# Performance work log

Measured on AMD Instinct MI355X. Metric: run time of the kernel, lower is better.

The kernel has to match this reference:

```python
import jax, jax.numpy as jnp
import numpy as np

D_MODEL = 1024
D_FF = 2048
NA = 4
NB = 4
E = NA * NB
B = 2
S = 1024


def setup_inputs() -> dict:
    key = jax.random.key(0)
    ks = jax.random.split(key, 8)
    s = 0.02
    x = jax.random.normal(ks[0], (B, S, D_MODEL), dtype=jnp.float32)
    # stacked per-expert FFN params (torch Linear stored as [in, out] here)
    W1 = (jax.random.normal(ks[1], (E, D_MODEL, 2 * D_FF), dtype=jnp.float32) * s)
    b1 = jnp.zeros((E, 2 * D_FF), dtype=jnp.float32)
    W2 = (jax.random.normal(ks[2], (E, D_FF, D_MODEL), dtype=jnp.float32) * s)
    b2 = jnp.zeros((E, D_MODEL), dtype=jnp.float32)
    Wga = jax.random.normal(ks[3], (D_MODEL, NA), dtype=jnp.float32) * s
    bga = jnp.zeros((NA,), dtype=jnp.float32)
    Wgb = jax.random.normal(ks[4], (D_MODEL, NB), dtype=jnp.float32) * s
    bgb = jnp.zeros((NB,), dtype=jnp.float32)
    return {"x": x, "W1": W1, "b1": b1, "W2": W2, "b2": b2,
            "Wga": Wga, "bga": bga, "Wgb": Wgb, "bgb": bgb}


def reference(x, W1, b1, W2, b2, Wga, bga, Wgb, bgb):
    b, s, d = x.shape
    xf = x.reshape(b * s, d)                     # [T, d]
    probs_A = jax.nn.softmax(xf @ Wga + bga, axis=-1)   # [T, NA]
    probs_B = jax.nn.softmax(xf @ Wgb + bgb, axis=-1)   # [T, NB]
    idx_A = jnp.argmax(probs_A, axis=-1)
    idx_B = jnp.argmax(probs_B, axis=-1)
    oh_A = jax.nn.one_hot(idx_A, NA, dtype=xf.dtype)
    oh_B = jax.nn.one_hot(idx_B, NB, dtype=xf.dtype)
    aux_A = NA * jnp.sum(probs_A.mean(0) * oh_A.mean(0))
    aux_B = NB * jnp.sum(probs_B.mean(0) * oh_B.mean(0))
    total_aux = aux_A + aux_B

    # flattened Cartesian expert index per token
    e_idx = idx_A * NB + idx_B                   # [T]

    # run all experts densely, then select per token (vectorized dispatch)
    h = jnp.einsum('td,edf->etf', xf, W1) + b1[:, None, :]   # [E, T, 2*d_ff]
    a, g = jnp.split(h, 2, axis=-1)
    act = a * jax.nn.silu(g)                                  # [E, T, d_ff]
    y = jnp.einsum('etf,efd->etd', act, W2) + b2[:, None, :]  # [E, T, d]
    oh_E = jax.nn.one_hot(e_idx, E, dtype=xf.dtype)           # [T, E]
    out = jnp.einsum('te,etd->td', oh_E, y)                   # [T, d]
    return out.reshape(b, s, d), total_aux
```

## Files before the change

kernel.cpp:

```cpp
#include <hip/hip_runtime.h>
#include <cstdint>
#include <cstddef>

#define TOKENS 2048
#define DM 1024
#define DFF 2048
#define HC 4096
#define NE 16
#define BM 128

typedef __bf16 bf16x8 __attribute__((ext_vector_type(8)));
typedef float floatx4 __attribute__((ext_vector_type(4)));

static __device__ __forceinline__ unsigned short f2bf(float f) {
    union { float f; unsigned int u; } v; v.f = f;
    unsigned int r = v.u + 0x7fffu + ((v.u >> 16) & 1u);
    return (unsigned short)(r >> 16);
}

union BF8 { bf16x8 v; unsigned short u[8]; };

__global__ __launch_bounds__(256) void moe_gating(
    const float* __restrict__ x, const float* __restrict__ Wga, const float* __restrict__ bga,
    const float* __restrict__ Wgb, const float* __restrict__ bgb,
    float* __restrict__ probsA, float* __restrict__ probsB, int* __restrict__ e_idx)
{
    int wv = threadIdx.x >> 6, lane = threadIdx.x & 63;
    int t = blockIdx.x * 4 + wv;
    const float* xr = x + (size_t)t * DM;
    double aA[4] = {0.,0.,0.,0.}, aB[4] = {0.,0.,0.,0.};
    for (int k = lane; k < DM; k += 64) {
        double xv = (double)xr[k];
        float4 wa = *(const float4*)(Wga + k * 4);
        float4 wb = *(const float4*)(Wgb + k * 4);
        aA[0] += xv * wa.x; aA[1] += xv * wa.y; aA[2] += xv * wa.z; aA[3] += xv * wa.w;
        aB[0] += xv * wb.x; aB[1] += xv * wb.y; aB[2] += xv * wb.z; aB[3] += xv * wb.w;
    }
    #pragma unroll
    for (int off = 32; off >= 1; off >>= 1) {
        #pragma unroll
        for (int j = 0; j < 4; ++j) {
            aA[j] += __shfl_xor(aA[j], off);
            aB[j] += __shfl_xor(aB[j], off);
        }
    }
    if (lane == 0) {
        double lA[4], lB[4];
        #pragma unroll
        for (int j = 0; j < 4; ++j) {
            lA[j] = aA[j] + (double)bga[j];
            lB[j] = aB[j] + (double)bgb[j];
        }
        int ia = 0, ib = 0;
        #pragma unroll
        for (int j = 1; j < 4; ++j) {
            if (lA[j] > lA[ia]) ia = j;
            if (lB[j] > lB[ib]) ib = j;
        }
        double sA = 0., sB = 0., pA[4], pB[4];
        #pragma unroll
        for (int j = 0; j < 4; ++j) {
            pA[j] = exp(lA[j] - lA[ia]); sA += pA[j];
            pB[j] = exp(lB[j] - lB[ib]); sB += pB[j];
        }
        float4 oa, ob;
        oa.x = (float)(pA[0]/sA); oa.y = (float)(pA[1]/sA);
        oa.z = (float)(pA[2]/sA); oa.w = (float)(pA[3]/sA);
        ob.x = (float)(pB[0]/sB); ob.y = (float)(pB[1]/sB);
        ob.z = (float)(pB[2]/sB); ob.w = (float)(pB[3]/sB);
        *(float4*)(probsA + t * 4) = oa;
        *(float4*)(probsB + t * 4) = ob;
        e_idx[t] = ia * 4 + ib;
    }
}

__global__ __launch_bounds__(256) void moe_stats(
    const float* __restrict__ probsA, const float* __restrict__ probsB,
    const int* __restrict__ e_idx,
    int* __restrict__ countE, int* __restrict__ offsets, float* __restrict__ aux_out)
{
    __shared__ float sA[4], sB[4];
    __shared__ int cA[4], cB[4], cE[16];
    int tid = threadIdx.x;
    if (tid < 4) { sA[tid] = 0.f; sB[tid] = 0.f; cA[tid] = 0; cB[tid] = 0; }
    if (tid < 16) cE[tid] = 0;
    __syncthreads();
    float lA[4] = {0,0,0,0}, lB[4] = {0,0,0,0};
    for (int t = tid; t < TOKENS; t += 256) {
        float4 pa = *(const float4*)(probsA + t * 4);
        float4 pb = *(const float4*)(probsB + t * 4);
        lA[0] += pa.x; lA[1] += pa.y; lA[2] += pa.z; lA[3] += pa.w;
        lB[0] += pb.x; lB[1] += pb.y; lB[2] += pb.z; lB[3] += pb.w;
        int e = e_idx[t];
        atomicAdd(&cE[e], 1);
        atomicAdd(&cA[e >> 2], 1);
        atomicAdd(&cB[e & 3], 1);
    }
    #pragma unroll
    for (int j = 0; j < 4; ++j) {
        atomicAdd(&sA[j], lA[j]);
        atomicAdd(&sB[j], lB[j]);
    }
    __syncthreads();
    if (tid == 0) {
        int acc = 0;
        for (int e = 0; e < NE; ++e) { offsets[e] = acc; countE[e] = cE[e]; acc += cE[e]; }
        offsets[NE] = acc;
        float invT = 1.0f / (float)TOKENS;
        float auxA = 0.f, auxB = 0.f;
        for (int j = 0; j < 4; ++j) {
            auxA += (sA[j] * invT) * ((float)cA[j] * invT);
            auxB += (sB[j] * invT) * ((float)cB[j] * invT);
        }
        aux_out[0] = 4.0f * auxA + 4.0f * auxB;
    }
}

__global__ __launch_bounds__(256) void moe_slot(const int* __restrict__ e_idx,
                                                const int* __restrict__ offsets,
                                                int* __restrict__ cursor, int* __restrict__ perm)
{
    int t = blockIdx.x * 256 + threadIdx.x;
    int e = e_idx[t];
    int s = offsets[e] + atomicAdd(&cursor[e], 1);
    perm[s] = t;
}

__global__ __launch_bounds__(256) void moe_gather(const float* __restrict__ x,
                                                  const int* __restrict__ perm,
                                                  unsigned short* __restrict__ Xg)
{
    int s = blockIdx.x;
    int t = perm[s];
    int i = threadIdx.x * 4;
    float4 v = *(const float4*)(x + (size_t)t * DM + i);
    ushort4 o;
    o.x = f2bf(v.x); o.y = f2bf(v.y); o.z = f2bf(v.z); o.w = f2bf(v.w);
    *(ushort4*)(Xg + (size_t)s * DM + i) = o;
}

__global__ __launch_bounds__(256) void moe_ffn1(
    const unsigned short* __restrict__ Xg, const float* __restrict__ W1,
    const float* __restrict__ b1, const int* __restrict__ countE,
    const int* __restrict__ offsets, unsigned short* __restrict__ actbuf)
{
    int e = blockIdx.y;
    int cnt = countE[e];
    if (cnt == 0) return;
    int base = offsets[e];
    int n0 = blockIdx.x * 64;
    __shared__ __align__(16) unsigned short Xs[2 * BM * 40];
    int tid = threadIdx.x, wv = tid >> 6, lane = tid & 63;
    int quad = lane >> 4, l15 = lane & 15;
    const float* W1e = W1 + (size_t)e * DM * HC;
    int col = n0 + wv * 16 + l15;
    const float* pa = W1e + col;
    const float* pg = W1e + DFF + col;
    float ba = b1[e * HC + col];
    float bg = b1[e * HC + DFF + col];
    int row = tid >> 2, kc = tid & 3;

    for (int m0 = blockIdx.z * BM; m0 < cnt; m0 += 2 * BM) {
        floatx4 acc[8][2];
        #pragma unroll
        for (int i = 0; i < 8; ++i) {
            acc[i][0] = floatx4{0.f,0.f,0.f,0.f};
            acc[i][1] = floatx4{0.f,0.f,0.f,0.f};
        }
        #pragma unroll
        for (int p = 0; p < 2; ++p) {
            int r = row + p * 64;
            uint4 v = {0u,0u,0u,0u};
            int m = m0 + r;
            if (m < cnt) v = *(const uint4*)(Xg + (size_t)(base + m) * DM + kc * 8);
            *(uint4*)(Xs + r * 40 + kc * 8) = v;
        }
        float curA[8], curG[8], nxtA[8], nxtG[8];
        {
            const float* qa = pa + (size_t)(quad * 8) * HC;
            const float* qg = pg + (size_t)(quad * 8) * HC;
            #pragma unroll
            for (int j = 0; j < 8; ++j) { curA[j] = qa[(size_t)j * HC]; curG[j] = qg[(size_t)j * HC]; }
        }
        __syncthreads();
        for (int ks = 0; ks < DM / 32; ++ks) {
            int buf = ks & 1;
            if (ks + 1 < DM / 32) {
                int k0n = (ks + 1) * 32;
                #pragma unroll
                for (int p = 0; p < 2; ++p) {
                    int r = row + p * 64;
                    uint4 v = {0u,0u,0u,0u};
                    int m = m0 + r;
                    if (m < cnt) v = *(const uint4*)(Xg + (size_t)(base + m) * DM + k0n + kc * 8);
                    *(uint4*)(Xs + (buf ^ 1) * (BM * 40) + r * 40 + kc * 8) = v;
                }
            }
            bf16x8 af[8];
            #pragma unroll
            for (int i = 0; i < 8; ++i)
                af[i] = *(const bf16x8*)(Xs + buf * (BM * 40) + (i * 16 + l15) * 40 + quad * 8);
            if (ks + 1 < DM / 32) {
                const float* qa = pa + (size_t)((ks + 1) * 32 + quad * 8) * HC;
                const float* qg = pg + (size_t)((ks + 1) * 32 + quad * 8) * HC;
                #pragma unroll
                for (int j = 0; j < 8; ++j) { nxtA[j] = qa[(size_t)j * HC]; nxtG[j] = qg[(size_t)j * HC]; }
            }
            BF8 fa, fg;
            #pragma unroll
            for (int j = 0; j < 8; ++j) { fa.u[j] = f2bf(curA[j]); fg.u[j] = f2bf(curG[j]); }
            #pragma unroll
            for (int i = 0; i < 8; ++i) {
                acc[i][0] = __builtin_amdgcn_mfma_f32_16x16x32_bf16(af[i], fa.v, acc[i][0], 0, 0, 0);
                acc[i][1] = __builtin_amdgcn_mfma_f32_16x16x32_bf16(af[i], fg.v, acc[i][1], 0, 0, 0);
            }
            #pragma unroll
            for (int j = 0; j < 8; ++j) { curA[j] = nxtA[j]; curG[j] = nxtG[j]; }
            __syncthreads();
        }
        #pragma unroll
        for (int i = 0; i < 8; ++i) {
            #pragma unroll
            for (int r = 0; r < 4; ++r) {
                int mr = m0 + i * 16 + quad * 4 + r;
                if (mr < cnt) {
                    float a = acc[i][0][r] + ba;
                    float g = acc[i][1][r] + bg;
                    float sg = 1.0f / (1.0f + __expf(-g));
                    actbuf[(size_t)(base + mr) * DFF + col] = f2bf(a * (g * sg));
                }
            }
        }
    }
}

__global__ __launch_bounds__(256) void moe_ffn2(
    const unsigned short* __restrict__ actbuf, const float* __restrict__ W2,
    const float* __restrict__ b2, const int* __restrict__ countE,
    const int* __restrict__ offsets, const int* __restrict__ perm,
    float* __restrict__ out)
{
    int e = blockIdx.y;
    int cnt = countE[e];
    if (cnt == 0) return;
    int base = offsets[e];
    int n0 = blockIdx.x * 64;
    __shared__ __align__(16) unsigned short As[2 * BM * 40];
    int tid = threadIdx.x, wv = tid >> 6, lane = tid & 63;
    int quad = lane >> 4, l15 = lane & 15;
    const float* W2e = W2 + (size_t)e * DFF * DM;
    int col = n0 + wv * 16 + l15;
    const float* pb = W2e + col;
    float bias = b2[e * DM + col];
    int row = tid >> 2, kc = tid & 3;

    for (int m0 = blockIdx.z * BM; m0 < cnt; m0 += 2 * BM) {
        floatx4 acc[8];
        #pragma unroll
        for (int i = 0; i < 8; ++i) acc[i] = floatx4{0.f,0.f,0.f,0.f};
        #pragma unroll
        for (int p = 0; p < 2; ++p) {
            int r = row + p * 64;
            uint4 v = {0u,0u,0u,0u};
            int m = m0 + r;
            if (m < cnt) v = *(const uint4*)(actbuf + (size_t)(base + m) * DFF + kc * 8);
            *(uint4*)(As + r * 40 + kc * 8) = v;
        }
        float curB[8], nxtB[8];
        {
            const float* qb = pb + (size_t)(quad * 8) * DM;
            #pragma unroll
            for (int j = 0; j < 8; ++j) curB[j] = qb[(size_t)j * DM];
        }
        __syncthreads();
        for (int ks = 0; ks < DFF / 32; ++ks) {
            int buf = ks & 1;
            if (ks + 1 < DFF / 32) {
                int k0n = (ks + 1) * 32;
                #pragma unroll
                for (int p = 0; p < 2; ++p) {
                    int r = row + p * 64;
                    uint4 v = {0u,0u,0u,0u};
                    int m = m0 + r;
                    if (m < cnt) v = *(const uint4*)(actbuf + (size_t)(base + m) * DFF + k0n + kc * 8);
                    *(uint4*)(As + (buf ^ 1) * (BM * 40) + r * 40 + kc * 8) = v;
                }
            }
            bf16x8 af[8];
            #pragma unroll
            for (int i = 0; i < 8; ++i)
                af[i] = *(const bf16x8*)(As + buf * (BM * 40) + (i * 16 + l15) * 40 + quad * 8);
            if (ks + 1 < DFF / 32) {
                const float* qb = pb + (size_t)((ks + 1) * 32 + quad * 8) * DM;
                #pragma unroll
                for (int j = 0; j < 8; ++j) nxtB[j] = qb[(size_t)j * DM];
            }
            BF8 fb;
            #pragma unroll
            for (int j = 0; j < 8; ++j) fb.u[j] = f2bf(curB[j]);
            #pragma unroll
            for (int i = 0; i < 8; ++i)
                acc[i] = __builtin_amdgcn_mfma_f32_16x16x32_bf16(af[i], fb.v, acc[i], 0, 0, 0);
            #pragma unroll
            for (int j = 0; j < 8; ++j) curB[j] = nxtB[j];
            __syncthreads();
        }
        #pragma unroll
        for (int i = 0; i < 8; ++i) {
            #pragma unroll
            for (int r = 0; r < 4; ++r) {
                int mr = m0 + i * 16 + quad * 4 + r;
                if (mr < cnt) {
                    int t = perm[base + mr];
                    out[(size_t)t * DM + col] = acc[i][r] + bias;
                }
            }
        }
    }
}

extern "C" void kernel_launch(void* const* d_in, const int* in_sizes, int n_in,
                              void* d_out, int out_size, void* d_ws, size_t ws_size,
                              hipStream_t stream)
{
    (void)in_sizes; (void)n_in; (void)out_size; (void)ws_size;
    const float* x   = (const float*)d_in[0];
    const float* W1  = (const float*)d_in[1];
    const float* b1  = (const float*)d_in[2];
    const float* W2  = (const float*)d_in[3];
    const float* b2  = (const float*)d_in[4];
    const float* Wga = (const float*)d_in[5];
    const float* bga = (const float*)d_in[6];
    const float* Wgb = (const float*)d_in[7];
    const float* bgb = (const float*)d_in[8];
    float* out = (float*)d_out;

    char* ws = (char*)d_ws;
    int*   countE  = (int*)(ws + 0);
    int*   cursor  = (int*)(ws + 64);
    int*   offsets = (int*)(ws + 256);
    int*   e_idx   = (int*)(ws + 512);
    int*   perm    = (int*)(ws + 8704);
    float* probsA  = (float*)(ws + 16896);
    float* probsB  = (float*)(ws + 49664);
    unsigned short* Xg     = (unsigned short*)(ws + 131072);
    unsigned short* actbuf = (unsigned short*)(ws + (size_t)8 * 1024 * 1024);

    hipMemsetAsync(ws, 0, 256, stream);
    moe_gating<<<TOKENS / 4, 256, 0, stream>>>(x, Wga, bga, Wgb, bgb,
                                               probsA, probsB, e_idx);
    moe_stats<<<1, 256, 0, stream>>>(probsA, probsB, e_idx, countE, offsets,
                                     out + (size_t)TOKENS * DM);
    moe_slot<<<TOKENS / 256, 256, 0, stream>>>(e_idx, offsets, cursor, perm);
    moe_gather<<<TOKENS, 256, 0, stream>>>(x, perm, Xg);
    moe_ffn1<<<dim3(DFF / 64, NE, 2), 256, 0, stream>>>(Xg, W1, b1, countE, offsets, actbuf);
    moe_ffn2<<<dim3(DM / 64, NE, 2), 256, 0, stream>>>(actbuf, W2, b2, countE, offsets, perm, out);
}
```

Before: 579.4 us.

## Pre-swizzle activations into MFMA fragment layout and drop LDS staging in FFN kernels

Token rows are padded per expert to multiples of 16, and the gather writes bf16 activations directly in the per-lane MFMA A-fragment order. The FFN kernels then load A fragments straight from global memory with no shared-memory staging or barriers. FFN1 also writes its output in the same fragment layout for FFN2. The slot kernel and the memset are folded into the stats kernel. Tiles change to 32 columns with two M-waves per block, which doubles the number of blocks along N but removes the z split, so W is reread more from L2.

```diff
diff --git a/kernel.cpp b/kernel.cpp
--- a/kernel.cpp
+++ b/kernel.cpp
@@ -7,7 +7,7 @@
 #define DFF 2048
 #define HC 4096
 #define NE 16
-#define BM 128
+#define PADROWS 2560
 
 typedef __bf16 bf16x8 __attribute__((ext_vector_type(8)));
 typedef float floatx4 __attribute__((ext_vector_type(4)));
@@ -77,13 +77,14 @@
 __global__ __launch_bounds__(256) void moe_stats(
     const float* __restrict__ probsA, const float* __restrict__ probsB,
     const int* __restrict__ e_idx,
-    int* __restrict__ countE, int* __restrict__ offsets, float* __restrict__ aux_out)
+    int* __restrict__ countE, int* __restrict__ offsetsP, int* __restrict__ perm,
+    float* __restrict__ aux_out)
 {
     __shared__ float sA[4], sB[4];
-    __shared__ int cA[4], cB[4], cE[16];
+    __shared__ int cA[4], cB[4], cE[16], cur[16], offS[16];
     int tid = threadIdx.x;
     if (tid < 4) { sA[tid] = 0.f; sB[tid] = 0.f; cA[tid] = 0; cB[tid] = 0; }
-    if (tid < 16) cE[tid] = 0;
+    if (tid < 16) { cE[tid] = 0; cur[tid] = 0; }
     __syncthreads();
     float lA[4] = {0,0,0,0}, lB[4] = {0,0,0,0};
     for (int t = tid; t < TOKENS; t += 256) {
@@ -104,8 +105,11 @@
     __syncthreads();
     if (tid == 0) {
         int acc = 0;
-        for (int e = 0; e < NE; ++e) { offsets[e] = acc; countE[e] = cE[e]; acc += cE[e]; }
-        offsets[NE] = acc;
+        for (int e = 0; e < NE; ++e) {
+            offS[e] = acc; offsetsP[e] = acc; countE[e] = cE[e];
+            acc += (cE[e] + 15) & ~15;
+        }
+        offsetsP[NE] = acc;
         float invT = 1.0f / (float)TOKENS;
         float auxA = 0.f, auxB = 0.f;
         for (int j = 0; j < 4; ++j) {
@@ -114,92 +118,78 @@
         }
         aux_out[0] = 4.0f * auxA + 4.0f * auxB;
     }
-}
-
-__global__ __launch_bounds__(256) void moe_slot(const int* __restrict__ e_idx,
-                                                const int* __restrict__ offsets,
-                                                int* __restrict__ cursor, int* __restrict__ perm)
-{
-    int t = blockIdx.x * 256 + threadIdx.x;
-    int e = e_idx[t];
-    int s = offsets[e] + atomicAdd(&cursor[e], 1);
-    perm[s] = t;
+    __syncthreads();
+    for (int s = tid; s < PADROWS; s += 256) perm[s] = 0;
+    __syncthreads();
+    for (int t = tid; t < TOKENS; t += 256) {
+        int e = e_idx[t];
+        int s = offS[e] + atomicAdd(&cur[e], 1);
+        perm[s] = t;
+    }
 }
 
 __global__ __launch_bounds__(256) void moe_gather(const float* __restrict__ x,
                                                   const int* __restrict__ perm,
-                                                  unsigned short* __restrict__ Xg)
-{
-    int s = blockIdx.x;
-    int t = perm[s];
-    int i = threadIdx.x * 4;
-    float4 v = *(const float4*)(x + (size_t)t * DM + i);
-    ushort4 o;
-    o.x = f2bf(v.x); o.y = f2bf(v.y); o.z = f2bf(v.z); o.w = f2bf(v.w);
-    *(ushort4*)(Xg + (size_t)s * DM + i) = o;
+                                                  unsigned short* __restrict__ Xg2)
+{
+    int g = blockIdx.x;
+    int wv = threadIdx.x >> 6, lane = threadIdx.x & 63;
+    int r = lane & 15, ko = (lane >> 4) * 8;
+    int t = perm[g * 16 + r];
+    const float* xr = x + (size_t)t * DM;
+    for (int c = wv; c < DM / 32; c += 4) {
+        int k = c * 32 + ko;
+        float4 v0 = *(const float4*)(xr + k);
+        float4 v1 = *(const float4*)(xr + k + 4);
+        BF8 o;
+        o.u[0] = f2bf(v0.x); o.u[1] = f2bf(v0.y); o.u[2] = f2bf(v0.z); o.u[3] = f2bf(v0.w);
+        o.u[4] = f2bf(v1.x); o.u[5] = f2bf(v1.y); o.u[6] = f2bf(v1.z); o.u[7] = f2bf(v1.w);
+        *(bf16x8*)(Xg2 + ((size_t)(g * (DM / 32) + c) * 64 + lane) * 8) = o.v;
+    }
 }
 
 __global__ __launch_bounds__(256) void moe_ffn1(
-    const unsigned short* __restrict__ Xg, const float* __restrict__ W1,
+    const unsigned short* __restrict__ Xg2, const float* __restrict__ W1,
     const float* __restrict__ b1, const int* __restrict__ countE,
-    const int* __restrict__ offsets, unsigned short* __restrict__ actbuf)
+    const int* __restrict__ offsetsP, unsigned short* __restrict__ actbuf2)
 {
     int e = blockIdx.y;
     int cnt = countE[e];
     if (cnt == 0) return;
-    int base = offsets[e];
-    int n0 = blockIdx.x * 64;
-    __shared__ __align__(16) unsigned short Xs[2 * BM * 40];
+    int baseP = offsetsP[e];
     int tid = threadIdx.x, wv = tid >> 6, lane = tid & 63;
+    int wn = wv & 1, wm = wv >> 1;
     int quad = lane >> 4, l15 = lane & 15;
+    int n0 = blockIdx.x * 32;
+    int col = n0 + wn * 16 + l15;
     const float* W1e = W1 + (size_t)e * DM * HC;
-    int col = n0 + wv * 16 + l15;
     const float* pa = W1e + col;
     const float* pg = W1e + DFF + col;
     float ba = b1[e * HC + col];
     float bg = b1[e * HC + DFF + col];
-    int row = tid >> 2, kc = tid & 3;
-
-    for (int m0 = blockIdx.z * BM; m0 < cnt; m0 += 2 * BM) {
+    int colHi = col >> 5, colSw = 16 * ((col >> 3) & 3), colLo = col & 7;
+
+    for (int m0 = wm * 128; m0 < cnt; m0 += 256) {
+        int sg0 = (baseP >> 4) + (m0 >> 4);
         floatx4 acc[8][2];
         #pragma unroll
         for (int i = 0; i < 8; ++i) {
             acc[i][0] = floatx4{0.f,0.f,0.f,0.f};
             acc[i][1] = floatx4{0.f,0.f,0.f,0.f};
         }
-        #pragma unroll
-        for (int p = 0; p < 2; ++p) {
-            int r = row + p * 64;
-            uint4 v = {0u,0u,0u,0u};
-            int m = m0 + r;
-            if (m < cnt) v = *(const uint4*)(Xg + (size_t)(base + m) * DM + kc * 8);
-            *(uint4*)(Xs + r * 40 + kc * 8) = v;
-        }
-        float curA[8], curG[8], nxtA[8], nxtG[8];
+        float curA[8], curG[8];
         {
             const float* qa = pa + (size_t)(quad * 8) * HC;
             const float* qg = pg + (size_t)(quad * 8) * HC;
             #pragma unroll
             for (int j = 0; j < 8; ++j) { curA[j] = qa[(size_t)j * HC]; curG[j] = qg[(size_t)j * HC]; }
         }
-        __syncthreads();
         for (int ks = 0; ks < DM / 32; ++ks) {
-            int buf = ks & 1;
-            if (ks + 1 < DM / 32) {
-                int k0n = (ks + 1) * 32;
-                #pragma unroll
-                for (int p = 0; p < 2; ++p) {
-                    int r = row + p * 64;
-                    uint4 v = {0u,0u,0u,0u};
-                    int m = m0 + r;
-                    if (m < cnt) v = *(const uint4*)(Xg + (size_t)(base + m) * DM + k0n + kc * 8);
-                    *(uint4*)(Xs + (buf ^ 1) * (BM * 40) + r * 40 + kc * 8) = v;
-                }
-            }
             bf16x8 af[8];
             #pragma unroll
             for (int i = 0; i < 8; ++i)
-                af[i] = *(const bf16x8*)(Xs + buf * (BM * 40) + (i * 16 + l15) * 40 + quad * 8);
+                af[i] = *(const bf16x8*)(Xg2 + ((size_t)((sg0 + i) * (DM / 32) + ks) * 64 + lane) * 8);
+            float nxtA[8], nxtG[8];
             if (ks + 1 < DM / 32) {
                 const float* qa = pa + (size_t)((ks + 1) * 32 + quad * 8) * HC;
                 const float* qg = pg + (size_t)((ks + 1) * 32 + quad * 8) * HC;
@@ -216,7 +206,6 @@
             }
             #pragma unroll
             for (int j = 0; j < 8; ++j) { curA[j] = nxtA[j]; curG[j] = nxtG[j]; }
-            __syncthreads();
         }
         #pragma unroll
         for (int i = 0; i < 8; ++i) {
@@ -227,7 +216,9 @@
                     float a = acc[i][0][r] + ba;
                     float g = acc[i][1][r] + bg;
                     float sg = 1.0f / (1.0f + __expf(-g));
-                    actbuf[(size_t)(base + mr) * DFF + col] = f2bf(a * (g * sg));
+                    size_t a8 = ((size_t)((sg0 + i) * (DFF / 32) + colHi) * 64
+                                 + (quad * 4 + r) + colSw);
+                    actbuf2[a8 * 8 + colLo] = f2bf(a * (g * sg));
                 }
             }
         }
@@ -235,61 +226,41 @@
 }
 
 __global__ __launch_bounds__(256) void moe_ffn2(
-    const unsigned short* __restrict__ actbuf, const float* __restrict__ W2,
+    const unsigned short* __restrict__ actbuf2, const float* __restrict__ W2,
     const float* __restrict__ b2, const int* __restrict__ countE,
-    const int* __restrict__ offsets, const int* __restrict__ perm,
+    const int* __restrict__ offsetsP, const int* __restrict__ perm,
     float* __restrict__ out)
 {
     int e = blockIdx.y;
     int cnt = countE[e];
     if (cnt == 0) return;
-    int base = offsets[e];
-    int n0 = blockIdx.x * 64;
-    __shared__ __align__(16) unsigned short As[2 * BM * 40];
+    int baseP = offsetsP[e];
     int tid = threadIdx.x, wv = tid >> 6, lane = tid & 63;
+    int wn = wv & 1, wm = wv >> 1;
     int quad = lane >> 4, l15 = lane & 15;
+    int n0 = blockIdx.x * 32;
+    int col = n0 + wn * 16 + l15;
     const float* W2e = W2 + (size_t)e * DFF * DM;
-    int col = n0 + wv * 16 + l15;
     const float* pb = W2e + col;
     float bias = b2[e * DM + col];
-    int row = tid >> 2, kc = tid & 3;
-
-    for (int m0 = blockIdx.z * BM; m0 < cnt; m0 += 2 * BM) {
+
+    for (int m0 = wm * 128; m0 < cnt; m0 += 256) {
+        int sg0 = (baseP >> 4) + (m0 >> 4);
         floatx4 acc[8];
         #pragma unroll
         for (int i = 0; i < 8; ++i) acc[i] = floatx4{0.f,0.f,0.f,0.f};
-        #pragma unroll
-        for (int p = 0; p < 2; ++p) {
-            int r = row + p * 64;
-            uint4 v = {0u,0u,0u,0u};
-            int m = m0 + r;
-            if (m < cnt) v = *(const uint4*)(actbuf + (size_t)(base + m) * DFF + kc * 8);
-            *(uint4*)(As + r * 40 + kc * 8) = v;
-        }
-        float curB[8], nxtB[8];
+        float curB[8];
         {
             const float* qb = pb + (size_t)(quad * 8) * DM;
             #pragma unroll
             for (int j = 0; j < 8; ++j) curB[j] = qb[(size_t)j * DM];
         }
-        __syncthreads();
         for (int ks = 0; ks < DFF / 32; ++ks) {
-            int buf = ks & 1;
-            if (ks + 1 < DFF / 32) {
-                int k0n = (ks + 1) * 32;
-                #pragma unroll
-                for (int p = 0; p < 2; ++p) {
-                    int r = row + p * 64;
-                    uint4 v = {0u,0u,0u,0u};
-                    int m = m0 + r;
-                    if (m < cnt) v = *(const uint4*)(actbuf + (size_t)(base + m) * DFF + k0n + kc * 8);
-                    *(uint4*)(As + (buf ^ 1) * (BM * 40) + r * 40 + kc * 8) = v;
-                }
-            }
             bf16x8 af[8];
             #pragma unroll
             for (int i = 0; i < 8; ++i)
-                af[i] = *(const bf16x8*)(As + buf * (BM * 40) + (i * 16 + l15) * 40 + quad * 8);
+                af[i] = *(const bf16x8*)(actbuf2 + ((size_t)((sg0 + i) * (DFF / 32) + ks) * 64 + lane) * 8);
+            float nxtB[8];
             if (ks + 1 < DFF / 32) {
                 const float* qb = pb + (size_t)((ks + 1) * 32 + quad * 8) * DM;
                 #pragma unroll
@@ -303,7 +274,6 @@
                 acc[i] = __builtin_amdgcn_mfma_f32_16x16x32_bf16(af[i], fb.v, acc[i], 0, 0, 0);
             #pragma unroll
             for (int j = 0; j < 8; ++j) curB[j] = nxtB[j];
-            __syncthreads();
         }
         #pragma unroll
         for (int i = 0; i < 8; ++i) {
@@ -311,7 +281,7 @@
             for (int r = 0; r < 4; ++r) {
                 int mr = m0 + i * 16 + quad * 4 + r;
                 if (mr < cnt) {
-                    int t = perm[base + mr];
+                    int t = perm[baseP + mr];
                     out[(size_t)t * DM + col] = acc[i][r] + bias;
                 }
             }
@@ -336,23 +306,20 @@
     float* out = (float*)d_out;
 
     char* ws = (char*)d_ws;
-    int*   countE  = (int*)(ws + 0);
-    int*   cursor  = (int*)(ws + 64);
-    int*   offsets = (int*)(ws + 256);
-    int*   e_idx   = (int*)(ws + 512);
-    int*   perm    = (int*)(ws + 8704);
-    float* probsA  = (float*)(ws + 16896);
-    float* probsB  = (float*)(ws + 49664);
-    unsigned short* Xg     = (unsigned short*)(ws + 131072);
-    unsigned short* actbuf = (unsigned short*)(ws + (size_t)8 * 1024 * 1024);
-
-    hipMemsetAsync(ws, 0, 256, stream);
+    int*   countE   = (int*)(ws + 0);
+    int*   offsetsP = (int*)(ws + 64);
+    int*   e_idx    = (int*)(ws + 256);
+    float* probsA   = (float*)(ws + 16384);
+    float* probsB   = (float*)(ws + 49152);
+    int*   perm     = (int*)(ws + 81920);
+    unsigned short* Xg2     = (unsigned short*)(ws + (size_t)1 * 1024 * 1024);
+    unsigned short* actbuf2 = (unsigned short*)(ws + (size_t)6 * 1024 * 1024);
+
     moe_gating<<<TOKENS / 4, 256, 0, stream>>>(x, Wga, bga, Wgb, bgb,
                                                probsA, probsB, e_idx);
-    moe_stats<<<1, 256, 0, stream>>>(probsA, probsB, e_idx, countE, offsets,
+    moe_stats<<<1, 256, 0, stream>>>(probsA, probsB, e_idx, countE, offsetsP, perm,
                                      out + (size_t)TOKENS * DM);
-    moe_slot<<<TOKENS / 256, 256, 0, stream>>>(e_idx, offsets, cursor, perm);
-    moe_gather<<<TOKENS, 256, 0, stream>>>(x, perm, Xg);
-    moe_ffn1<<<dim3(DFF / 64, NE, 2), 256, 0, stream>>>(Xg, W1, b1, countE, offsets, actbuf);
-    moe_ffn2<<<dim3(DM / 64, NE, 2), 256, 0, stream>>>(actbuf, W2, b2, countE, offsets, perm, out);
-}
+    moe_gather<<<PADROWS / 16, 256, 0, stream>>>(x, perm, Xg2);
+    moe_ffn1<<<dim3(DFF / 32, NE), 256, 0, stream>>>(Xg2, W1, b1, countE, offsetsP, actbuf2);
+    moe_ffn2<<<dim3(DM / 32, NE), 256, 0, stream>>>(actbuf2, W2, b2, countE, offsetsP, perm, out);
+}
```

Measured after the change: 594.3 us. +2.6%, slower.
